# Optimization experiments

Measured on AMD Instinct MI355X. Metric: run time of the kernel, lower is better.

## Reference

```python
import jax, jax.numpy as jnp
import numpy as np
import math

HEAD_DIM = 64
HEAD_NUM = 8  # hidden_dim(512) // head_dim(64)
EPS = 1e-8


def modulated_linear(x, s, weight, aff_w, aff_b):
    # x: [B, N, IN], s: [B, S], weight: [OUT, IN], aff_w: [IN, S], aff_b: [IN]
    style = s @ aff_w.T + aff_b                       # [B, IN]
    w = weight[None, :, :] * style[:, None, :]        # [B, OUT, IN]
    demod = jax.lax.rsqrt(jnp.sum(w * w, axis=2) + EPS)  # [B, OUT]
    w = w * demod[:, :, None]
    return jnp.einsum('bni,boi->bno', x, w)           # [B, N, OUT]


def setup_inputs() -> dict:
    key = jax.random.key(0)
    ks = jax.random.split(key, 8)
    B, N, F, S = 8, 1024, 512, 512
    sc = 1.0 / math.sqrt(F)
    return {
        'x': jax.random.normal(ks[0], (B, N, F), dtype=jnp.float32),
        's': jax.random.normal(ks[1], (B, S), dtype=jnp.float32),
        'k_weight': jax.random.normal(ks[2], (F, F), dtype=jnp.float32) * sc,
        'k_aff_w': jax.random.normal(ks[3], (F, S), dtype=jnp.float32) * sc,
        'k_aff_b': jnp.ones((F,), dtype=jnp.float32),
        'o_weight': jax.random.normal(ks[4], (F, F), dtype=jnp.float32) * sc,
        'o_aff_w': jax.random.normal(ks[5], (F, S), dtype=jnp.float32) * sc,
        'o_aff_b': jnp.ones((F,), dtype=jnp.float32),
    }


def reference(x, s, k_weight, k_aff_w, k_aff_b, o_weight, o_aff_w, o_aff_b):
    B, N, _ = x.shape
    # Original code computes q, k, v all via k_mapping (faithful to the bug).
    kqv = modulated_linear(x, s, k_weight, k_aff_w, k_aff_b)  # [B, N, hidden]
    kqv = kqv.reshape(B, N, HEAD_NUM, HEAD_DIM)               # [B, N, H, D]
    q = k = v = kqv
    scale = 1.0 / math.sqrt(HEAD_DIM)
    scores = jnp.einsum('bnhd,bmhd->bhnm', q, k) * scale      # [B, H, N, N]
    attn = jax.nn.softmax(scores, axis=-1)
    out = jnp.einsum('bhnm,bmhd->bnhd', attn, v)              # [B, N, H, D]
    out = out.reshape(B, N, HEAD_NUM * HEAD_DIM)
    return modulated_linear(out, s, o_weight, o_aff_w, o_aff_b)
```

## Files before the change

kernel.cpp:

```cpp
#include <hip/hip_runtime.h>
#include <stdint.h>

using short8  = __attribute__((ext_vector_type(8))) short;
using f32x4   = __attribute__((ext_vector_type(4))) float;
using float4v = __attribute__((ext_vector_type(4))) float;
using u16x4   = __attribute__((ext_vector_type(4))) unsigned short;

__device__ __forceinline__ unsigned short f2b(float f) {
    union { float f; unsigned int i; } v; v.f = f;
    unsigned int i = v.i;
    unsigned int r = (i + 0x7fffu + ((i >> 16) & 1u)) >> 16;
    return (unsigned short)r;
}
__device__ __forceinline__ short8 ld8(const unsigned short* p) {
    return *reinterpret_cast<const short8*>(p);
}
__device__ __forceinline__ void st8(unsigned short* p, short8 v) {
    *reinterpret_cast<short8*>(p) = v;
}
__device__ __forceinline__ f32x4 mfma16(short8 a, short8 b, f32x4 c) {
    return __builtin_amdgcn_mfma_f32_16x16x32_bf16(a, b, c, 0, 0, 0);
}
__device__ __forceinline__ void stC(float* p, float v)          { *p = v; }
__device__ __forceinline__ void stC(unsigned short* p, float v) { *p = f2b(v); }

__device__ __forceinline__ void gl16(const unsigned short* g, unsigned short* l) {
    __builtin_amdgcn_global_load_lds(
        (const __attribute__((address_space(1))) void*)g,
        (__attribute__((address_space(3))) void*)l,
        16, 0, 0);
}

__device__ __forceinline__ unsigned int cvtpk(float lo, float hi) {
    unsigned int r;
    asm("v_cvt_pk_bf16_f32 %0, %1, %2" : "=v"(r) : "v"(lo), "v"(hi));
    return r;
}
__device__ __forceinline__ void pl32swap(unsigned int& a, unsigned int& b) {
    asm("v_permlane32_swap_b32 %0, %1" : "+v"(a), "+v"(b));
}
__device__ __forceinline__ void pl16swap(unsigned int& a, unsigned int& b) {
    asm("v_permlane16_swap_b32 %0, %1" : "+v"(a), "+v"(b));
}
__device__ __forceinline__ short8 pack4(unsigned int x0, unsigned int x1,
                                        unsigned int x2, unsigned int x3) {
    union { unsigned int u[4]; short8 s; } c;
    c.u[0] = x0; c.u[1] = x1; c.u[2] = x2; c.u[3] = x3;
    return c.s;
}

__global__ __launch_bounds__(256) void cvt_kernel(
    const float* __restrict__ x, unsigned short* __restrict__ xb)
{
    int i = (blockIdx.x * 256 + threadIdx.x) * 8;
    float4v v0 = *reinterpret_cast<const float4v*>(x + i);
    float4v v1 = *reinterpret_cast<const float4v*>(x + i + 4);
    short8 o;
#pragma unroll
    for (int j = 0; j < 4; ++j) o[j] = (short)f2b(v0[j]);
#pragma unroll
    for (int j = 0; j < 4; ++j) o[4 + j] = (short)f2b(v1[j]);
    st8(xb + i, o);
}

__global__ __launch_bounds__(256) void style_kernel(
    const float* __restrict__ s,
    const float* __restrict__ k_aff_w, const float* __restrict__ k_aff_b,
    const float* __restrict__ o_aff_w, const float* __restrict__ o_aff_b,
    float* __restrict__ style)
{
    int wid  = blockIdx.x * 4 + (threadIdx.x >> 6);
    int lane = threadIdx.x & 63;
    int map  = wid >> 12;
    int rem  = wid & 4095;
    int b    = rem >> 9;
    int i    = rem & 511;
    const float* aw = map ? o_aff_w : k_aff_w;
    const float* ab = map ? o_aff_b : k_aff_b;
    const float* sp = s  + b * 512 + lane * 8;
    const float* wp = aw + i * 512 + lane * 8;
    float acc = 0.f;
#pragma unroll
    for (int j = 0; j < 8; ++j) acc += sp[j] * wp[j];
#pragma unroll
    for (int off = 1; off < 64; off <<= 1) acc += __shfl_xor(acc, off, 64);
    if (lane == 0) style[(map * 8 + b) * 512 + i] = acc + ab[i];
}

__global__ __launch_bounds__(256) void modw_kernel(
    const float* __restrict__ k_weight,
    const float* __restrict__ o_weight,
    const float* __restrict__ style,
    unsigned short* __restrict__ wmod)
{
    int wid  = blockIdx.x * 4 + (threadIdx.x >> 6);
    int lane = threadIdx.x & 63;
    int map  = wid >> 12;
    int rem  = wid & 4095;
    int b    = rem >> 9;
    int o    = rem & 511;
    const float* wrow = (map ? o_weight : k_weight) + o * 512 + lane * 8;
    const float* st   = style + (map * 8 + b) * 512 + lane * 8;
    float w[8]; float ss = 0.f;
#pragma unroll
    for (int j = 0; j < 8; ++j) { w[j] = wrow[j] * st[j]; ss += w[j] * w[j]; }
#pragma unroll
    for (int off = 1; off < 64; off <<= 1) ss += __shfl_xor(ss, off, 64);
    float demod = rsqrtf(ss + 1e-8f);
    short8 ov;
#pragma unroll
    for (int j = 0; j < 8; ++j) ov[j] = (short)f2b(w[j] * demod);
    unsigned short* dst = wmod + (((size_t)map * 8 + b) * 512 + o) * 512 + lane * 8;
    *reinterpret_cast<short8*>(dst) = ov;
}

template <typename CT, bool WVT>
__global__ __launch_bounds__(256) void gemm_bt_lds_kernel(
    const unsigned short* __restrict__ A,
    const unsigned short* __restrict__ Bt,
    CT* __restrict__ C,
    unsigned short* __restrict__ VT)
{
    __shared__ __align__(16) unsigned short smem[4 * 4096];

    int blk = blockIdx.x;
    int b   = blk & 7;
    int rem = blk >> 3;
    int mt  = rem & 15;
    int nt  = rem >> 4;
    int tid  = threadIdx.x;
    int w    = tid >> 6;
    int lane = tid & 63;
    int quad = lane >> 4;
    int r    = lane & 15;
    int wm   = w >> 1;
    int wn   = w & 1;

    const unsigned short* Ab = A  + ((size_t)b * 1024 + mt * 64) * 512;
    const unsigned short* Bb = Bt + ((size_t)b * 512  + nt * 64) * 512;

    int lrow = lane >> 3;
    int lunit = (lane & 7) ^ lrow;
    int laneoff = lrow * 512 + lunit * 8;

    f32x4 acc[2][2];
#pragma unroll
    for (int i = 0; i < 2; ++i)
#pragma unroll
        for (int j = 0; j < 2; ++j) acc[i][j] = f32x4{0.f, 0.f, 0.f, 0.f};

    auto stage = [&](int sbuf, int kt) {
        int ko = kt * 64;
        unsigned short* Asb = smem + sbuf * 4096;
        unsigned short* Bsb = smem + 8192 + sbuf * 4096;
#pragma unroll
        for (int c = 0; c < 2; ++c) {
            int chunk = w * 2 + c;
            gl16(Ab + (size_t)chunk * 8 * 512 + laneoff + ko, Asb + chunk * 512);
            gl16(Bb + (size_t)chunk * 8 * 512 + laneoff + ko, Bsb + chunk * 512);
        }
    };
    auto frag = [&](int row, int kh) {
        return row * 64 + ((((kh << 2) | quad) ^ (row & 7)) << 3);
    };

    stage(0, 0);
    __syncthreads();

#pragma unroll
    for (int ks = 0; ks < 8; ++ks) {
        int s = ks & 1;
        if (ks < 7) stage(s ^ 1, ks + 1);
        const unsigned short* Ap = smem + s * 4096;
        const unsigned short* Bp = smem + 8192 + s * 4096;
#pragma unroll
        for (int kh = 0; kh < 2; ++kh) {
            short8 af[2], bf[2];
#pragma unroll
            for (int i = 0; i < 2; ++i)
                af[i] = ld8(Ap + frag(wm * 32 + i * 16 + r, kh));
#pragma unroll
            for (int j = 0; j < 2; ++j)
                bf[j] = ld8(Bp + frag(wn * 32 + j * 16 + r, kh));
#pragma unroll
            for (int i = 0; i < 2; ++i)
#pragma unroll
                for (int j = 0; j < 2; ++j)
                    acc[i][j] = mfma16(af[i], bf[j], acc[i][j]);
        }
        __syncthreads();
    }

    CT* Cb = C + (size_t)b * 1024 * 512;
#pragma unroll
    for (int i = 0; i < 2; ++i)
#pragma unroll
        for (int rr = 0; rr < 4; ++rr) {
            int row = mt * 64 + wm * 32 + i * 16 + quad * 4 + rr;
#pragma unroll
            for (int j = 0; j < 2; ++j) {
                int col = nt * 64 + wn * 32 + j * 16 + r;
                stC(Cb + (size_t)row * 512 + col, acc[i][j][rr]);
            }
        }
    if (WVT) {
        constexpr int TP = 72;
        unsigned short (*Tt)[TP] = reinterpret_cast<unsigned short (*)[TP]>(smem);
#pragma unroll
        for (int i = 0; i < 2; ++i)
#pragma unroll
            for (int j = 0; j < 2; ++j) {
                int d = wn * 32 + j * 16 + r;
#pragma unroll
                for (int rh = 0; rh < 2; ++rh) {
                    int tok = wm * 32 + i * 16 + quad * 4 + rh * 2;
                    unsigned int pv = (unsigned int)f2b(acc[i][j][rh * 2]) |
                                      ((unsigned int)f2b(acc[i][j][rh * 2 + 1]) << 16);
                    *reinterpret_cast<unsigned int*>(&Tt[d][tok]) = pv;
                }
            }
        __syncthreads();
        int d  = tid >> 2;
        int cc = tid & 3;
        const unsigned short* src = &Tt[d][cc * 16];
        unsigned short* dst = VT + ((size_t)(b * 8 + nt) * 64 + d) * 1024 + mt * 64 + cc * 16;
        short8 t0 = ld8(src), t1 = ld8(src + 8);
        st8(dst,     t0);
        st8(dst + 8, t1);
    }
}

__global__ __launch_bounds__(256) void attn_kernel(
    const unsigned short* __restrict__ kqv,
    const unsigned short* __restrict__ vt,
    unsigned short* __restrict__ attn_out)
{
    constexpr int PAD = 72;
    int blk = blockIdx.x;
    int bh = blk & 63;
    int qt = blk >> 6;
    int b  = bh >> 3, h = bh & 7;
    int tid  = threadIdx.x;
    int lane = tid & 63;
    int quad = lane >> 4;
    int r    = lane & 15;

    __shared__ __align__(16) unsigned short klds[2][64][PAD];
    __shared__ __align__(16) unsigned short vlds[2][64][PAD];

    const unsigned short* Mb = kqv + (size_t)b * 1024 * 512;
    int wv = tid >> 6;
    int q0 = qt * 64 + wv * 16;

    const unsigned short* qptr = Mb + (size_t)(q0 + r) * 512 + h * 64 + quad * 8;
    short8 bq0 = ld8(qptr);
    short8 bq1 = ld8(qptr + 32);

    short8 ones;
#pragma unroll
    for (int j = 0; j < 8; ++j) ones[j] = (short)0x3F80;

    f32x4 o0 = {0.f, 0.f, 0.f, 0.f};
    f32x4 o1 = o0, o2 = o0, o3 = o0, lacc = o0;

    int srow0 = tid >> 3;
    int srow1 = srow0 + 32;
    int scol  = (tid & 7) * 8;
    const unsigned short* Kg = Mb + h * 64;
    const unsigned short* Vg = vt + (size_t)bh * 64 * 1024;

    {
        short8 k0v = ld8(Kg + (size_t)srow0 * 512 + scol);
        short8 k1v = ld8(Kg + (size_t)srow1 * 512 + scol);
        short8 v0v = ld8(Vg + (size_t)srow0 * 1024 + scol);
        short8 v1v = ld8(Vg + (size_t)srow1 * 1024 + scol);
        st8(&klds[0][srow0][scol], k0v);
        st8(&klds[0][srow1][scol], k1v);
        st8(&vlds[0][srow0][scol], v0v);
        st8(&vlds[0][srow1][scol], v1v);
    }
    __syncthreads();

    const float c  = 0.18033688011112042f;
    const float CM = 28.853900817779268f;

    for (int it = 0; it < 16; ++it) {
        int s = it & 1;
        short8 pk0, pk1, pv0, pv1;
        if (it < 15) {
            int k0n = (it + 1) * 64;
            pk0 = ld8(Kg + (size_t)(k0n + srow0) * 512 + scol);
            pk1 = ld8(Kg + (size_t)(k0n + srow1) * 512 + scol);
            pv0 = ld8(Vg + (size_t)srow0 * 1024 + k0n + scol);
            pv1 = ld8(Vg + (size_t)srow1 * 1024 + k0n + scol);
        }
        f32x4 st_[4];
#pragma unroll
        for (int t = 0; t < 4; ++t) {
            short8 ka = ld8(&klds[s][t * 16 + r][quad * 8]);
            short8 kb = ld8(&klds[s][t * 16 + r][32 + quad * 8]);
            f32x4 sacc = {0.f, 0.f, 0.f, 0.f};
            sacc = mfma16(ka, bq0, sacc);
            sacc = mfma16(kb, bq1, sacc);
            st_[t] = sacc;
        }
        unsigned int pk_[4][2];
#pragma unroll
        for (int t = 0; t < 4; ++t)
#pragma unroll
            for (int h2 = 0; h2 < 2; ++h2)
                pk_[t][h2] = cvtpk(exp2f(st_[t][2 * h2]     * c - CM),
                                   exp2f(st_[t][2 * h2 + 1] * c - CM));
        unsigned int a0 = pk_[0][0], b0 = pk_[1][0];
        pl32swap(a0, b0); pl16swap(a0, b0);
        unsigned int a1 = pk_[0][1], b1 = pk_[1][1];
        pl32swap(a1, b1); pl16swap(a1, b1);
        unsigned int c0 = pk_[2][0], d0 = pk_[3][0];
        pl32swap(c0, d0); pl16swap(c0, d0);
        unsigned int c1 = pk_[2][1], d1 = pk_[3][1];
        pl32swap(c1, d1); pl16swap(c1, d1);
        short8 ap0 = pack4(a0, a1, b0, b1);
        short8 ap1 = pack4(c0, c1, d0, d1);
        {
            short8 va, vb;
            va = ld8(&vlds[s][0 * 16 + r][quad * 8]);
            vb = ld8(&vlds[s][0 * 16 + r][32 + quad * 8]);
            o0 = mfma16(ap0, va, o0);  o0 = mfma16(ap1, vb, o0);
            va = ld8(&vlds[s][1 * 16 + r][quad * 8]);
            vb = ld8(&vlds[s][1 * 16 + r][32 + quad * 8]);
            o1 = mfma16(ap0, va, o1);  o1 = mfma16(ap1, vb, o1);
            va = ld8(&vlds[s][2 * 16 + r][quad * 8]);
            vb = ld8(&vlds[s][2 * 16 + r][32 + quad * 8]);
            o2 = mfma16(ap0, va, o2);  o2 = mfma16(ap1, vb, o2);
            va = ld8(&vlds[s][3 * 16 + r][quad * 8]);
            vb = ld8(&vlds[s][3 * 16 + r][32 + quad * 8]);
            o3 = mfma16(ap0, va, o3);  o3 = mfma16(ap1, vb, o3);
            lacc = mfma16(ap0, ones, lacc);
            lacc = mfma16(ap1, ones, lacc);
        }
        if (it < 15) {
            int ns = s ^ 1;
            st8(&klds[ns][srow0][scol], pk0);
            st8(&klds[ns][srow1][scol], pk1);
            st8(&vlds[ns][srow0][scol], pv0);
            st8(&vlds[ns][srow1][scol], pv1);
        }
        __syncthreads();
    }

    unsigned short* ob = attn_out + (size_t)b * 1024 * 512 + (size_t)h * 64;
#pragma unroll
    for (int rr = 0; rr < 4; ++rr) {
        float inv = 1.0f / lacc[rr];
        int n = q0 + quad * 4 + rr;
        unsigned short* orow = ob + (size_t)n * 512 + r;
        orow[0]  = f2b(o0[rr] * inv);
        orow[16] = f2b(o1[rr] * inv);
        orow[32] = f2b(o2[rr] * inv);
        orow[48] = f2b(o3[rr] * inv);
    }
}

extern "C" void kernel_launch(void* const* d_in, const int* in_sizes, int n_in,
                              void* d_out, int out_size, void* d_ws, size_t ws_size,
                              hipStream_t stream)
{
    const float* x        = (const float*)d_in[0];
    const float* s        = (const float*)d_in[1];
    const float* k_weight = (const float*)d_in[2];
    const float* k_aff_w  = (const float*)d_in[3];
    const float* k_aff_b  = (const float*)d_in[4];
    const float* o_weight = (const float*)d_in[5];
    const float* o_aff_w  = (const float*)d_in[6];
    const float* o_aff_b  = (const float*)d_in[7];
    float* out = (float*)d_out;

    char* ws = (char*)d_ws;
    float* style          = (float*)ws;
    unsigned short* wmod  = (unsigned short*)(ws + 32 * 1024);
    unsigned short* attn  = wmod + (size_t)2 * 8 * 512 * 512;
    unsigned short* kqv   = attn + (size_t)8 * 1024 * 512;
    unsigned short* vt    = kqv  + (size_t)8 * 1024 * 512;
    unsigned short* xb    = vt   + (size_t)64 * 64 * 1024;

    cvt_kernel  <<<2048, 256, 0, stream>>>(x, xb);
    style_kernel<<<2048, 256, 0, stream>>>(s, k_aff_w, k_aff_b, o_aff_w, o_aff_b, style);
    modw_kernel <<<2048, 256, 0, stream>>>(k_weight, o_weight, style, wmod);
    gemm_bt_lds_kernel<unsigned short, true><<<1024, 256, 0, stream>>>(xb, wmod, kqv, vt);
    attn_kernel<<<1024, 256, 0, stream>>>(kqv, vt, attn);
    gemm_bt_lds_kernel<float, false><<<1024, 256, 0, stream>>>(attn, wmod + (size_t)8 * 512 * 512, out, nullptr);
}
```

Measured before the change: 140.8 us.

## Process two 16-row query tiles per wave in attention to reuse K/V LDS tiles

Each wave in the attention kernel now handles 32 query rows as two 16-row subtiles, sharing every K and V fragment loaded from LDS between both. The query tile per block doubles to 128 rows and the grid halves to 512 blocks. The aim is to halve global-to-LDS K/V traffic and LDS reads per unit of MFMA work. In exchange, register pressure roughly doubles and there are fewer blocks (2 per CU on 256 CUs), which lowers occupancy and latency hiding.

```diff
diff --git a/kernel.cpp b/kernel.cpp
--- a/kernel.cpp
+++ b/kernel.cpp
@@ -250,18 +250,20 @@
 
     const unsigned short* Mb = kqv + (size_t)b * 1024 * 512;
     int wv = tid >> 6;
-    int q0 = qt * 64 + wv * 16;
-
-    const unsigned short* qptr = Mb + (size_t)(q0 + r) * 512 + h * 64 + quad * 8;
-    short8 bq0 = ld8(qptr);
-    short8 bq1 = ld8(qptr + 32);
+    int q0 = qt * 128 + wv * 32;
+
+    const unsigned short* qpA = Mb + (size_t)(q0 + r) * 512 + h * 64 + quad * 8;
+    const unsigned short* qpB = Mb + (size_t)(q0 + 16 + r) * 512 + h * 64 + quad * 8;
+    short8 aq0 = ld8(qpA), aq1 = ld8(qpA + 32);
+    short8 cq0 = ld8(qpB), cq1 = ld8(qpB + 32);
 
     short8 ones;
 #pragma unroll
     for (int j = 0; j < 8; ++j) ones[j] = (short)0x3F80;
 
-    f32x4 o0 = {0.f, 0.f, 0.f, 0.f};
-    f32x4 o1 = o0, o2 = o0, o3 = o0, lacc = o0;
+    f32x4 z = {0.f, 0.f, 0.f, 0.f};
+    f32x4 oA0 = z, oA1 = z, oA2 = z, oA3 = z, lA = z;
+    f32x4 oB0 = z, oB1 = z, oB2 = z, oB3 = z, lB = z;
 
     int srow0 = tid >> 3;
     int srow1 = srow0 + 32;
@@ -284,26 +286,7 @@
     const float c  = 0.18033688011112042f;
     const float CM = 28.853900817779268f;
 
-    for (int it = 0; it < 16; ++it) {
-        int s = it & 1;
-        short8 pk0, pk1, pv0, pv1;
-        if (it < 15) {
-            int k0n = (it + 1) * 64;
-            pk0 = ld8(Kg + (size_t)(k0n + srow0) * 512 + scol);
-            pk1 = ld8(Kg + (size_t)(k0n + srow1) * 512 + scol);
-            pv0 = ld8(Vg + (size_t)srow0 * 1024 + k0n + scol);
-            pv1 = ld8(Vg + (size_t)srow1 * 1024 + k0n + scol);
-        }
-        f32x4 st_[4];
-#pragma unroll
-        for (int t = 0; t < 4; ++t) {
-            short8 ka = ld8(&klds[s][t * 16 + r][quad * 8]);
-            short8 kb = ld8(&klds[s][t * 16 + r][32 + quad * 8]);
-            f32x4 sacc = {0.f, 0.f, 0.f, 0.f};
-            sacc = mfma16(ka, bq0, sacc);
-            sacc = mfma16(kb, bq1, sacc);
-            st_[t] = sacc;
-        }
+    auto packP = [&](const f32x4* st_, short8& ap0, short8& ap1) {
         unsigned int pk_[4][2];
 #pragma unroll
         for (int t = 0; t < 4; ++t)
@@ -319,24 +302,53 @@
         pl32swap(c0, d0); pl16swap(c0, d0);
         unsigned int c1 = pk_[2][1], d1 = pk_[3][1];
         pl32swap(c1, d1); pl16swap(c1, d1);
-        short8 ap0 = pack4(a0, a1, b0, b1);
-        short8 ap1 = pack4(c0, c1, d0, d1);
+        ap0 = pack4(a0, a1, b0, b1);
+        ap1 = pack4(c0, c1, d0, d1);
+    };
+
+    for (int it = 0; it < 16; ++it) {
+        int s = it & 1;
+        short8 pk0, pk1, pv0, pv1;
+        if (it < 15) {
+            int k0n = (it + 1) * 64;
+            pk0 = ld8(Kg + (size_t)(k0n + srow0) * 512 + scol);
+            pk1 = ld8(Kg + (size_t)(k0n + srow1) * 512 + scol);
+            pv0 = ld8(Vg + (size_t)srow0 * 1024 + k0n + scol);
+            pv1 = ld8(Vg + (size_t)srow1 * 1024 + k0n + scol);
+        }
+        f32x4 sA[4], sB[4];
+#pragma unroll
+        for (int t = 0; t < 4; ++t) {
+            short8 ka = ld8(&klds[s][t * 16 + r][quad * 8]);
+            short8 kb = ld8(&klds[s][t * 16 + r][32 + quad * 8]);
+            f32x4 accA = z, accB = z;
+            accA = mfma16(ka, aq0, accA);  accA = mfma16(kb, aq1, accA);
+            accB = mfma16(ka, cq0, accB);  accB = mfma16(kb, cq1, accB);
+            sA[t] = accA;  sB[t] = accB;
+        }
+        short8 apA0, apA1, apB0, apB1;
+        packP(sA, apA0, apA1);
+        packP(sB, apB0, apB1);
         {
             short8 va, vb;
             va = ld8(&vlds[s][0 * 16 + r][quad * 8]);
             vb = ld8(&vlds[s][0 * 16 + r][32 + quad * 8]);
-            o0 = mfma16(ap0, va, o0);  o0 = mfma16(ap1, vb, o0);
+            oA0 = mfma16(apA0, va, oA0);  oA0 = mfma16(apA1, vb, oA0);
+            oB0 = mfma16(apB0, va, oB0);  oB0 = mfma16(apB1, vb, oB0);
             va = ld8(&vlds[s][1 * 16 + r][quad * 8]);
             vb = ld8(&vlds[s][1 * 16 + r][32 + quad * 8]);
-            o1 = mfma16(ap0, va, o1);  o1 = mfma16(ap1, vb, o1);
+            oA1 = mfma16(apA0, va, oA1);  oA1 = mfma16(apA1, vb, oA1);
+            oB1 = mfma16(apB0, va, oB1);  oB1 = mfma16(apB1, vb, oB1);
             va = ld8(&vlds[s][2 * 16 + r][quad * 8]);
             vb = ld8(&vlds[s][2 * 16 + r][32 + quad * 8]);
-            o2 = mfma16(ap0, va, o2);  o2 = mfma16(ap1, vb, o2);
+            oA2 = mfma16(apA0, va, oA2);  oA2 = mfma16(apA1, vb, oA2);
+            oB2 = mfma16(apB0, va, oB2);  oB2 = mfma16(apB1, vb, oB2);
             va = ld8(&vlds[s][3 * 16 + r][quad * 8]);
             vb = ld8(&vlds[s][3 * 16 + r][32 + quad * 8]);
-            o3 = mfma16(ap0, va, o3);  o3 = mfma16(ap1, vb, o3);
-            lacc = mfma16(ap0, ones, lacc);
-            lacc = mfma16(ap1, ones, lacc);
+            oA3 = mfma16(apA0, va, oA3);  oA3 = mfma16(apA1, vb, oA3);
+            oB3 = mfma16(apB0, va, oB3);  oB3 = mfma16(apB1, vb, oB3);
+            lA = mfma16(apA0, ones, lA);  lA = mfma16(apA1, ones, lA);
+            lB = mfma16(apB0, ones, lB);  lB = mfma16(apB1, ones, lB);
         }
         if (it < 15) {
             int ns = s ^ 1;
@@ -351,13 +363,20 @@
     unsigned short* ob = attn_out + (size_t)b * 1024 * 512 + (size_t)h * 64;
 #pragma unroll
     for (int rr = 0; rr < 4; ++rr) {
-        float inv = 1.0f / lacc[rr];
-        int n = q0 + quad * 4 + rr;
-        unsigned short* orow = ob + (size_t)n * 512 + r;
-        orow[0]  = f2b(o0[rr] * inv);
-        orow[16] = f2b(o1[rr] * inv);
-        orow[32] = f2b(o2[rr] * inv);
-        orow[48] = f2b(o3[rr] * inv);
+        float invA = 1.0f / lA[rr];
+        int nA = q0 + quad * 4 + rr;
+        unsigned short* orowA = ob + (size_t)nA * 512 + r;
+        orowA[0]  = f2b(oA0[rr] * invA);
+        orowA[16] = f2b(oA1[rr] * invA);
+        orowA[32] = f2b(oA2[rr] * invA);
+        orowA[48] = f2b(oA3[rr] * invA);
+        float invB = 1.0f / lB[rr];
+        int nB = q0 + 16 + quad * 4 + rr;
+        unsigned short* orowB = ob + (size_t)nB * 512 + r;
+        orowB[0]  = f2b(oB0[rr] * invB);
+        orowB[16] = f2b(oB1[rr] * invB);
+        orowB[32] = f2b(oB2[rr] * invB);
+        orowB[48] = f2b(oB3[rr] * invB);
     }
 }
 
@@ -387,6 +406,6 @@
     style_kernel<<<2048, 256, 0, stream>>>(s, k_aff_w, k_aff_b, o_aff_w, o_aff_b, style);
     modw_kernel <<<2048, 256, 0, stream>>>(k_weight, o_weight, style, wmod);
     gemm_bt_lds_kernel<unsigned short, true><<<1024, 256, 0, stream>>>(xb, wmod, kqv, vt);
-    attn_kernel<<<1024, 256, 0, stream>>>(kqv, vt, attn);
+    attn_kernel<<<512, 256, 0, stream>>>(kqv, vt, attn);
     gemm_bt_lds_kernel<float, false><<<1024, 256, 0, stream>>>(attn, wmod + (size_t)8 * 512 * 512, out, nullptr);
 }
```

After: 141.1 us, median of 2. Within noise of the previous version (+0.2%).
